# Optimization experiments

Hardware: AMD Instinct MI355X
Metric: run time of the kernel (lower is better)

The kernel has to match this reference:

```python
import jax, jax.numpy as jnp
import numpy as np

B, S, C = 2, 2048, 1024
U, H = 1024, 16
FFH = int(U * 4.0)
NEG = -1e9
EPS = 1e-5


def setup_inputs() -> dict:
    key = jax.random.key(0)
    ks = jax.random.split(key, 16)
    w = lambda k, sh: jax.random.normal(k, sh, dtype=jnp.float32) * 0.02
    return {
        'x': jax.random.normal(ks[0], (B, S, C), dtype=jnp.float32),
        'wq': w(ks[1], (C, U)), 'bq': jnp.zeros((U,), jnp.float32),
        'wk': w(ks[2], (C, U)), 'bk': jnp.zeros((U,), jnp.float32),
        'wv': w(ks[3], (C, U)), 'bv': jnp.zeros((U,), jnp.float32),
        'wf1': w(ks[4], (U, FFH)), 'bf1': jnp.zeros((FFH,), jnp.float32),
        'wf2': w(ks[5], (FFH, U)), 'bf2': jnp.zeros((U,), jnp.float32),
        'ln_g': jnp.ones((S, U), jnp.float32), 'ln_b': jnp.zeros((S, U), jnp.float32),
        'ffln_g': jnp.ones((S, U), jnp.float32), 'ffln_b': jnp.zeros((S, U), jnp.float32),
    }


def _ln2d(x, g, b):
    # LayerNorm over last two dims ([len_ts, units]) as in nn.LayerNorm([S, U])
    m = jnp.mean(x, axis=(-2, -1), keepdims=True)
    v = jnp.mean(jnp.square(x - m), axis=(-2, -1), keepdims=True)
    return (x - m) * jax.lax.rsqrt(v + EPS) * g + b


def reference(x, wq, bq, wk, bk, wv, bv, wf1, bf1, wf2, bf2, ln_g, ln_b, ffln_g, ffln_b):
    dh = U // H
    Q = (x @ wq + bq).reshape(B, S, H, dh)
    K = (x @ wk + bk).reshape(B, S, H, dh)
    V = (x @ wv + bv).reshape(B, S, H, dh)
    scores = jnp.einsum('bqhd,bkhd->bhqk', Q, K) / jnp.sqrt(jnp.float32(dh))
    mask = jnp.tril(jnp.ones((S, S), dtype=bool))  # causal tril buffer
    scores = jnp.where(mask, scores, NEG)
    attn = jax.nn.softmax(scores, axis=-1)
    out = jnp.einsum('bhqk,bkhd->bqhd', attn, V).reshape(B, S, U)
    out = out + x  # residual
    out = _ln2d(out, ln_g, ln_b)
    ff = jax.nn.relu(out @ wf1 + bf1) @ wf2 + bf2
    out = _ln2d(out + ff, ffln_g, ffln_b)
    return out
```

## Files before the change

kernel.cpp:

```cpp
#include <hip/hip_runtime.h>
#include <hip/hip_bf16.h>

typedef short s16x8 __attribute__((ext_vector_type(8)));
typedef float f32x4 __attribute__((ext_vector_type(4)));
typedef unsigned short u16x4 __attribute__((ext_vector_type(4)));

#define DEV static __device__ __forceinline__

DEV unsigned short f2bf(float f) {
  __hip_bfloat16 h = __float2bfloat16(f);
  return *reinterpret_cast<unsigned short*>(&h);
}
DEV float bf2f(unsigned short u) {
  union { unsigned u; float f; } v; v.u = (unsigned)u << 16; return v.f;
}

#define GLDS16(src, dst) \
  __builtin_amdgcn_global_load_lds((const __attribute__((address_space(1))) void*)(src), \
                                   (__attribute__((address_space(3))) void*)(dst), 16, 0, 0)

#define MFMA(a, b, c) __builtin_amdgcn_mfma_f32_16x16x32_bf16((a), (b), (c), 0, 0, 0)

__global__ __launch_bounds__(256) void k_f32_to_bf16(const float* __restrict__ in,
                                                     unsigned short* __restrict__ out, int n4) {
  int i = blockIdx.x * 256 + threadIdx.x;
  if (i >= n4) return;
  float4 v = ((const float4*)in)[i];
  u16x4 o; o.x = f2bf(v.x); o.y = f2bf(v.y); o.z = f2bf(v.z); o.w = f2bf(v.w);
  ((u16x4*)out)[i] = o;
}

__global__ __launch_bounds__(256) void k_transpose_w(const float* __restrict__ W,
                                                     unsigned short* __restrict__ Wt,
                                                     int K, int N, float scale) {
  __shared__ float t[64][65];
  int k0 = blockIdx.x * 64, n0 = blockIdx.y * 64;
  int tid = threadIdx.x;
#pragma unroll
  for (int i = 0; i < 16; ++i) {
    int idx = tid + i * 256; int r = idx >> 6, c = idx & 63;
    t[r][c] = W[(size_t)(k0 + r) * N + (n0 + c)];
  }
  __syncthreads();
#pragma unroll
  for (int i = 0; i < 16; ++i) {
    int idx = tid + i * 256; int r = idx >> 6, c = idx & 63;
    Wt[(size_t)(n0 + r) * K + (k0 + c)] = f2bf(t[c][r] * scale);
  }
}

__global__ void k_concat3(const float* __restrict__ a, const float* __restrict__ b,
                          const float* __restrict__ c, float* __restrict__ out, int n, float sa) {
  int i = blockIdx.x * 256 + threadIdx.x;
  if (i >= 3 * n) return;
  int j = (i < n) ? i : (i < 2 * n ? i - n : i - 2 * n);
  out[i] = (i < n) ? a[j] * sa : (i < 2 * n ? b[j] : c[j]);
}

template <int MODE>
__global__ __launch_bounds__(512, 2) void k_gemm8(
    const unsigned short* __restrict__ A, int lda,
    const unsigned short* __restrict__ Bt, int ldb,
    const float* __restrict__ bias,
    unsigned short* __restrict__ Cb, float* __restrict__ Cf, int ldc,
    int K, int nnt, size_t zstride) {
  __shared__ __align__(16) unsigned short As[2 * 2 * 8192];
  __shared__ __align__(16) unsigned short Bs[2 * 2 * 8192];
  int nwg = gridDim.x;
  int bid = blockIdx.x;
  int cpx = nwg >> 3;
  int swz = (bid & 7) * cpx + (bid >> 3);
  int mt = swz / nnt, nt = swz % nnt;
  int m0 = mt * 256, n0 = nt * 256;
  int tid = threadIdx.x, w = tid >> 6, l = tid & 63;
  int wm = (w >> 2) * 128, wn = (w & 3) * 64;
  int kb = blockIdx.z * K;

  int sr = tid >> 2;
  int gsrc = (tid & 3) ^ ((sr >> 1) & 3);
  const unsigned short* Ag0 = A + (size_t)(m0 + sr) * lda + kb + gsrc * 8;
  const unsigned short* Ag1 = Ag0 + (size_t)128 * lda;
  const unsigned short* Bg0 = Bt + (size_t)(n0 + sr) * ldb + kb + gsrc * 8;
  const unsigned short* Bg1 = Bg0 + (size_t)128 * ldb;

#define STG_A(t, kh) do { int _c = (t) * 64 + (kh) * 32; int _d = ((((t) & 1) * 2 + (kh)) * 8192); \
    GLDS16(Ag0 + _c, &As[_d + tid * 8]); GLDS16(Ag1 + _c, &As[_d + 4096 + tid * 8]); } while (0)
#define STG_B(t, kh) do { int _c = (t) * 64 + (kh) * 32; int _d = ((((t) & 1) * 2 + (kh)) * 8192); \
    GLDS16(Bg0 + _c, &Bs[_d + tid * 8]); GLDS16(Bg1 + _c, &Bs[_d + 4096 + tid * 8]); } while (0)

  int lswz = (l >> 1) & 3;
  int acol = ((l >> 4) ^ lswz) * 8;
  const unsigned short* Afr = &As[(wm + (l & 15)) * 32 + acol];
  const unsigned short* Bfr = &Bs[(wn + (l & 15)) * 32 + acol];

  f32x4 acc[8][4] = {};
  int nkt = K >> 6;

  STG_A(0, 0); STG_B(0, 0); STG_A(0, 1); STG_B(0, 1); STG_A(1, 0); STG_B(1, 0);
  asm volatile("s_waitcnt vmcnt(4)" ::: "memory");
  __builtin_amdgcn_s_barrier();
  __builtin_amdgcn_sched_barrier(0);

  for (int t = 0; t < nkt; ++t) {
    int cur = t & 1, rem = nkt - t;
    const unsigned short* ab = Afr + cur * 16384;
    const unsigned short* bb = Bfr + cur * 16384;
    s16x8 af[4], bf[4];
    if (t + 1 < nkt) STG_A(t + 1, 1);
#pragma unroll
    for (int nr = 0; nr < 4; ++nr) bf[nr] = *(const s16x8*)(bb + nr * 512);
#pragma unroll
    for (int mr = 0; mr < 4; ++mr) af[mr] = *(const s16x8*)(ab + mr * 512);
    __builtin_amdgcn_s_setprio(1);
#pragma unroll
    for (int mr = 0; mr < 4; ++mr)
#pragma unroll
      for (int nr = 0; nr < 4; ++nr)
        acc[mr][nr] = MFMA(af[mr], bf[nr], acc[mr][nr]);
    __builtin_amdgcn_s_setprio(0);
    if (t + 1 < nkt) STG_B(t + 1, 1);
#pragma unroll
    for (int mr = 0; mr < 4; ++mr) af[mr] = *(const s16x8*)(ab + 2048 + mr * 512);
    __builtin_amdgcn_s_setprio(1);
#pragma unroll
    for (int mr = 0; mr < 4; ++mr)
#pragma unroll
      for (int nr = 0; nr < 4; ++nr)
        acc[mr + 4][nr] = MFMA(af[mr], bf[nr], acc[mr + 4][nr]);
    __builtin_amdgcn_s_setprio(0);
    if (rem >= 2) { asm volatile("s_waitcnt vmcnt(4)" ::: "memory"); }
    else          { asm volatile("s_waitcnt vmcnt(0)" ::: "memory"); }
    __builtin_amdgcn_s_barrier();
    __builtin_amdgcn_sched_barrier(0);
    if (t + 2 < nkt) STG_A(t + 2, 0);
#pragma unroll
    for (int nr = 0; nr < 4; ++nr) bf[nr] = *(const s16x8*)(bb + 8192 + nr * 512);
#pragma unroll
    for (int mr = 0; mr < 4; ++mr) af[mr] = *(const s16x8*)(ab + 8192 + mr * 512);
    __builtin_amdgcn_s_setprio(1);
#pragma unroll
    for (int mr = 0; mr < 4; ++mr)
#pragma unroll
      for (int nr = 0; nr < 4; ++nr)
        acc[mr][nr] = MFMA(af[mr], bf[nr], acc[mr][nr]);
    __builtin_amdgcn_s_setprio(0);
    if (t + 2 < nkt) STG_B(t + 2, 0);
#pragma unroll
    for (int mr = 0; mr < 4; ++mr) af[mr] = *(const s16x8*)(ab + 8192 + 2048 + mr * 512);
    __builtin_amdgcn_s_setprio(1);
#pragma unroll
    for (int mr = 0; mr < 4; ++mr)
#pragma unroll
      for (int nr = 0; nr < 4; ++nr)
        acc[mr + 4][nr] = MFMA(af[mr], bf[nr], acc[mr + 4][nr]);
    __builtin_amdgcn_s_setprio(0);
    if (rem >= 3) { asm volatile("s_waitcnt vmcnt(4)" ::: "memory"); }
    else          { asm volatile("s_waitcnt vmcnt(0)" ::: "memory"); }
    __builtin_amdgcn_s_barrier();
    __builtin_amdgcn_sched_barrier(0);
  }
#undef STG_A
#undef STG_B

  unsigned short* Cbz = (MODE == 3) ? (Cb + zstride * blockIdx.z) : Cb;
#pragma unroll
  for (int mr = 0; mr < 8; ++mr) {
    int rb = m0 + wm + mr * 16 + (l >> 4) * 4;
#pragma unroll
    for (int nr = 0; nr < 4; ++nr) {
      int col = n0 + wn + nr * 16 + (l & 15);
      float bv = (MODE == 3) ? 0.f : bias[col];
#pragma unroll
      for (int j = 0; j < 4; ++j) {
        float v = acc[mr][nr][j] + bv;
        size_t off = (size_t)(rb + j) * ldc + col;
        if (MODE == 1) v = fmaxf(v, 0.f);
        Cbz[off] = f2bf(v);
      }
    }
  }
}

__global__ __launch_bounds__(256) void k_ff2_reduce(
    unsigned short* __restrict__ slices, const float* __restrict__ bias,
    const unsigned short* __restrict__ resid, float* __restrict__ partials) {
  __shared__ float red[8];
  int i = blockIdx.x;
  size_t rb = (size_t)i * 4096;
  int c = threadIdx.x * 4;
  u16x4 a0 = *(const u16x4*)(slices + rb + c);
  u16x4 a1 = *(const u16x4*)(slices + rb + 1024 + c);
  u16x4 a2 = *(const u16x4*)(slices + rb + 2048 + c);
  u16x4 a3 = *(const u16x4*)(slices + rb + 3072 + c);
  float4 bv = *(const float4*)(bias + c);
  u16x4 rv = *(const u16x4*)(resid + (size_t)i * 1024 + c);
  float4 o;
  o.x = bf2f(a0.x) + bf2f(a1.x) + bf2f(a2.x) + bf2f(a3.x) + bv.x + bf2f(rv.x);
  o.y = bf2f(a0.y) + bf2f(a1.y) + bf2f(a2.y) + bf2f(a3.y) + bv.y + bf2f(rv.y);
  o.z = bf2f(a0.z) + bf2f(a1.z) + bf2f(a2.z) + bf2f(a3.z) + bv.z + bf2f(rv.z);
  o.w = bf2f(a0.w) + bf2f(a1.w) + bf2f(a2.w) + bf2f(a3.w) + bv.w + bf2f(rv.w);
  __syncthreads();
  *(float4*)((float*)slices + (size_t)i * 2048 + c) = o;
  float bsum = o.x + o.y + o.z + o.w;
  float bsq = o.x * o.x + o.y * o.y + o.z * o.z + o.w * o.w;
  int wv = threadIdx.x >> 6, lv = threadIdx.x & 63;
#pragma unroll
  for (int mk = 1; mk < 64; mk <<= 1) { bsum += __shfl_xor(bsum, mk); bsq += __shfl_xor(bsq, mk); }
  if (lv == 0) { red[wv] = bsum; red[4 + wv] = bsq; }
  __syncthreads();
  if (threadIdx.x == 0) {
    partials[i * 2] = red[0] + red[1] + red[2] + red[3];
    partials[i * 2 + 1] = red[4] + red[5] + red[6] + red[7];
  }
}

__global__ __launch_bounds__(256) void k_transpose_v(const unsigned short* __restrict__ V, int ldv,
                                                     unsigned short* __restrict__ Vt, int S, int H) {
  __shared__ __align__(16) unsigned short t[64][72];
  int s0 = blockIdx.x * 64;
  int bh = blockIdx.y; int b = bh / H, h = bh % H;
  const unsigned short* src = V + (size_t)(b * S) * ldv + h * 64;
  unsigned short* dst = Vt + (size_t)bh * 64 * S;
  int tid = threadIdx.x;
#pragma unroll
  for (int i = 0; i < 2; ++i) {
    int idx = tid + i * 256;
    int s = idx >> 3, c = (idx & 7) * 8;
    s16x8 v = *(const s16x8*)(src + (size_t)(s0 + s) * ldv + c);
#pragma unroll
    for (int j = 0; j < 8; ++j) t[c + j][s] = (unsigned short)v[j];
  }
  __syncthreads();
#pragma unroll
  for (int i = 0; i < 2; ++i) {
    int idx = tid + i * 256;
    int d = idx >> 3, c = (idx & 7) * 8;
    *(s16x8*)(dst + (size_t)d * S + s0 + c) = *(const s16x8*)&t[d][c];
  }
}

__global__ __launch_bounds__(256) void k_attn(
    const unsigned short* __restrict__ Qg, const unsigned short* __restrict__ Kg,
    const unsigned short* __restrict__ Vt, int ldqk,
    const float* __restrict__ x, unsigned short* __restrict__ hpre,
    float* __restrict__ partials, int S, int H) {
  __shared__ __align__(16) unsigned short Ks[2][64 * 64];
  __shared__ __align__(16) unsigned short Vs[2][64 * 64];
  __shared__ __align__(16) unsigned short Ps[4][16 * 64];
  int bh = blockIdx.x, b = bh >> 4, h = bh & 15;
  const int nqt = S / 64;
  int qt = nqt - 1 - (int)blockIdx.y;
  int tid = threadIdx.x, w = tid >> 6, l = tid & 63;
  const int U = H * 64;
  const unsigned short* Qb = Qg + (size_t)(b * S) * ldqk + h * 64;
  const unsigned short* Kb = Kg + (size_t)(b * S) * ldqk + h * 64;
  const unsigned short* Vb = Vt + (size_t)bh * 64 * S;
  const float* xb = x + (size_t)(b * S) * U + h * 64;
  unsigned short* hb = hpre + (size_t)(b * S) * U + h * 64;
  int sg_r[2], sg_c[2];
#pragma unroll
  for (int it = 0; it < 2; ++it) {
    int g = it * 256 + tid;
    sg_r[it] = g >> 3;
    sg_c[it] = ((g & 7) ^ ((g >> 3) & 7)) * 8;
  }
  unsigned short* Pw = &Ps[w][0];
  int qloc = l & 15;
  int kloc = (l >> 4) * 4;

  int qrow = qt * 64 + w * 16 + qloc;
  s16x8 qf0 = *(const s16x8*)(Qb + (size_t)qrow * ldqk + (l >> 4) * 8);
  s16x8 qf1 = *(const s16x8*)(Qb + (size_t)qrow * ldqk + 32 + (l >> 4) * 8);
  f32x4 o[4] = {};
  float m = -1e30f, lsum = 0.f;

#pragma unroll
  for (int it = 0; it < 2; ++it) {
    GLDS16(Kb + (size_t)sg_r[it] * ldqk + sg_c[it], &Ks[0][(it * 256 + tid) * 8]);
    GLDS16(Vb + (size_t)sg_r[it] * S + sg_c[it], &Vs[0][(it * 256 + tid) * 8]);
  }

  for (int kt = 0; kt <= qt; ++kt) {
    int cur = kt & 1;
    __syncthreads();
    if (kt < qt) {
      int nb = cur ^ 1, kn = (kt + 1) * 64;
#pragma unroll
      for (int it = 0; it < 2; ++it) {
        GLDS16(Kb + (size_t)(kn + sg_r[it]) * ldqk + sg_c[it], &Ks[nb][(it * 256 + tid) * 8]);
        GLDS16(Vb + (size_t)sg_r[it] * S + kn + sg_c[it], &Vs[nb][(it * 256 + tid) * 8]);
      }
    }
    f32x4 sc[4];
    __builtin_amdgcn_s_setprio(1);
#pragma unroll
    for (int fn = 0; fn < 4; ++fn) {
      int row = fn * 16 + (l & 15);
      s16x8 kf0 = *(const s16x8*)&Ks[cur][row * 64 + ((((l >> 4)) ^ (row & 7)) * 8)];
      s16x8 kf1 = *(const s16x8*)&Ks[cur][row * 64 + (((4 + (l >> 4)) ^ (row & 7)) * 8)];
      f32x4 z = {};
      z = MFMA(kf0, qf0, z);
      z = MFMA(kf1, qf1, z);
      sc[fn] = z;
    }
    __builtin_amdgcn_s_setprio(0);
    if (kt == qt) {
      int qsel = w * 16 + qloc;
#pragma unroll
      for (int fn = 0; fn < 4; ++fn)
#pragma unroll
        for (int j = 0; j < 4; ++j)
          if (fn * 16 + kloc + j > qsel) sc[fn][j] = -1e30f;
    }
    float mx = sc[0][0];
#pragma unroll
    for (int fn = 0; fn < 4; ++fn)
#pragma unroll
      for (int j = 0; j < 4; ++j) mx = fmaxf(mx, sc[fn][j]);
    mx = fmaxf(mx, __shfl_xor(mx, 16));
    mx = fmaxf(mx, __shfl_xor(mx, 32));
    if (__ballot(mx > m + 11.5415603f)) {
      float mnew = fmaxf(m, mx);
      float alpha = exp2f(m - mnew);
      m = mnew;
      lsum *= alpha;
#pragma unroll
      for (int j = 0; j < 4; ++j) {
        float aj = __shfl(alpha, (l & 48) | (kloc + j));
#pragma unroll
        for (int fd = 0; fd < 4; ++fd) o[fd][j] *= aj;
      }
    }
    float rs = 0.f;
#pragma unroll
    for (int fn = 0; fn < 4; ++fn) {
      u16x4 pk;
#pragma unroll
      for (int j = 0; j < 4; ++j) {
        float p = exp2f(sc[fn][j] - m);
        rs += p;
        ((unsigned short*)&pk)[j] = f2bf(p);
      }
      int kb2 = fn * 16 + kloc;
      int el = qloc * 64 + (((kb2 >> 3) ^ (qloc & 7)) * 8) + (kb2 & 7);
      *(u16x4*)&Pw[el] = pk;
    }
    rs += __shfl_xor(rs, 16);
    rs += __shfl_xor(rs, 32);
    lsum += rs;
    __builtin_amdgcn_s_setprio(1);
#pragma unroll
    for (int kk = 0; kk < 2; ++kk) {
      int prow = l & 15;
      s16x8 pa = *(const s16x8*)&Pw[prow * 64 + (((kk * 4 + (l >> 4)) ^ (prow & 7)) * 8)];
#pragma unroll
      for (int fd = 0; fd < 4; ++fd) {
        int vrow = fd * 16 + (l & 15);
        s16x8 vf = *(const s16x8*)&Vs[cur][vrow * 64 + (((kk * 4 + (l >> 4)) ^ (vrow & 7)) * 8)];
        o[fd] = MFMA(pa, vf, o[fd]);
      }
    }
    __builtin_amdgcn_s_setprio(0);
  }
  float bsum = 0.f, bsq = 0.f;
#pragma unroll
  for (int j = 0; j < 4; ++j) {
    float lr = __shfl(lsum, (l & 48) | (kloc + j));
    float inv = 1.f / lr;
    int row = qt * 64 + w * 16 + kloc + j;
#pragma unroll
    for (int fd = 0; fd < 4; ++fd) {
      int col = fd * 16 + (l & 15);
      float v = o[fd][j] * inv + xb[(size_t)row * U + col];
      hb[(size_t)row * U + col] = f2bf(v);
      bsum += v; bsq += v * v;
    }
  }
#pragma unroll
  for (int mk = 1; mk < 64; mk <<= 1) { bsum += __shfl_xor(bsum, mk); bsq += __shfl_xor(bsq, mk); }
  if (l == 0) { float* r = (float*)&Ps[w][0]; r[0] = bsum; r[1] = bsq; }
  __syncthreads();
  if (tid == 0) {
    float s2 = 0.f, q2 = 0.f;
#pragma unroll
    for (int ww = 0; ww < 4; ++ww) { const float* r = (const float*)&Ps[ww][0]; s2 += r[0]; q2 += r[1]; }
    int pi = b * (H * nqt) + h * nqt + qt;
    partials[pi * 2] = s2; partials[pi * 2 + 1] = q2;
  }
}

__global__ __launch_bounds__(256) void k_ln_stats(const float* __restrict__ partials, int nper,
                                                  float* __restrict__ stats, float invN) {
  int b = blockIdx.x, tid = threadIdx.x;
  float s = 0.f, q = 0.f;
  for (int i = tid; i < nper; i += 256) { s += partials[(b * nper + i) * 2]; q += partials[(b * nper + i) * 2 + 1]; }
#pragma unroll
  for (int mk = 1; mk < 64; mk <<= 1) { s += __shfl_xor(s, mk); q += __shfl_xor(q, mk); }
  __shared__ float red[8];
  int w = tid >> 6, l = tid & 63;
  if (l == 0) { red[w] = s; red[4 + w] = q; }
  __syncthreads();
  if (tid == 0) {
    s = red[0] + red[1] + red[2] + red[3];
    q = red[4] + red[5] + red[6] + red[7];
    float m = s * invN, var = q * invN - m * m;
    stats[b * 2] = m; stats[b * 2 + 1] = rsqrtf(var + 1e-5f);
  }
}

__global__ __launch_bounds__(256) void k_ln_apply_b(
    const unsigned short* __restrict__ src, const float* __restrict__ stats,
    const float* __restrict__ g, const float* __restrict__ bt,
    unsigned short* __restrict__ outb, int SU) {
  int b = blockIdx.y;
  int idx = (blockIdx.x * 256 + threadIdx.x) * 4;
  float m = stats[b * 2], r = stats[b * 2 + 1];
  u16x4 v4 = *(const u16x4*)(src + (size_t)b * SU + idx);
  float4 gg = *(const float4*)(g + idx);
  float4 bb = *(const float4*)(bt + idx);
  u16x4 ob;
  ob.x = f2bf((bf2f(v4.x) - m) * r * gg.x + bb.x);
  ob.y = f2bf((bf2f(v4.y) - m) * r * gg.y + bb.y);
  ob.z = f2bf((bf2f(v4.z) - m) * r * gg.z + bb.z);
  ob.w = f2bf((bf2f(v4.w) - m) * r * gg.w + bb.w);
  *(u16x4*)(outb + (size_t)b * SU + idx) = ob;
}

__global__ __launch_bounds__(256) void k_ln_apply2(
    const float* __restrict__ src, const float* __restrict__ stats,
    const float* __restrict__ g, const float* __restrict__ bt,
    float* __restrict__ outf) {
  int b = blockIdx.y;
  int row = blockIdx.x;
  int grow = b * 2048 + row;
  int c = threadIdx.x * 4;
  float m = stats[b * 2], r = stats[b * 2 + 1];
  float4 v = *(const float4*)(src + (size_t)grow * 2048 + c);
  float4 gg = *(const float4*)(g + (size_t)row * 1024 + c);
  float4 bb = *(const float4*)(bt + (size_t)row * 1024 + c);
  float4 o;
  o.x = (v.x - m) * r * gg.x + bb.x;
  o.y = (v.y - m) * r * gg.y + bb.y;
  o.z = (v.z - m) * r * gg.z + bb.z;
  o.w = (v.w - m) * r * gg.w + bb.w;
  *(float4*)(outf + (size_t)grow * 1024 + c) = o;
}

extern "C" void kernel_launch(void* const* d_in, const int* in_sizes, int n_in,
                              void* d_out, int out_size, void* d_ws, size_t ws_size,
                              hipStream_t stream) {
  (void)in_sizes; (void)n_in; (void)out_size; (void)ws_size;
  const int S = 2048, H = 16;
  const float* x   = (const float*)d_in[0];
  const float* wq  = (const float*)d_in[1];
  const float* bq  = (const float*)d_in[2];
  const float* wk  = (const float*)d_in[3];
  const float* bk  = (const float*)d_in[4];
  const float* wv  = (const float*)d_in[5];
  const float* bv  = (const float*)d_in[6];
  const float* wf1 = (const float*)d_in[7];
  const float* bf1 = (const float*)d_in[8];
  const float* wf2 = (const float*)d_in[9];
  const float* bf2 = (const float*)d_in[10];
  const float* lng = (const float*)d_in[11];
  const float* lnb = (const float*)d_in[12];
  const float* ffg = (const float*)d_in[13];
  const float* ffb = (const float*)d_in[14];

  char* ws = (char*)d_ws;
  unsigned short* wqkvT = (unsigned short*)(ws);
  unsigned short* wf1T  = (unsigned short*)(ws + 6291456);
  unsigned short* wf2T  = (unsigned short*)(ws + 14680064);
  unsigned short* xb    = (unsigned short*)(ws + 23068672);
  unsigned short* qkv   = (unsigned short*)(ws + 31457280);
  unsigned short* vt    = (unsigned short*)(ws + 56623104);
  unsigned short* h1b   = (unsigned short*)(ws + 65011712);
  unsigned short* hpreb = (unsigned short*)(ws + 73400320);
  unsigned short* ff2s  = (unsigned short*)(ws + 73400320);
  unsigned short* f1b   = (unsigned short*)(ws + 23068672);
  float* biasqkv        = (float*)(ws + 106954752);
  float* part_attn      = (float*)(ws + 106967040);
  float* stats1         = (float*)(ws + 106977280);
  float* ffpart2        = (float*)(ws);
  float* stats2         = (float*)(ws + 65536);

  const float qscale = 0.125f * 1.44269504f;
  k_f32_to_bf16<<<4096, 256, 0, stream>>>(x, xb, 4096 * 1024 / 4);
  k_transpose_w<<<dim3(16, 16), 256, 0, stream>>>(wq, wqkvT, 1024, 1024, qscale);
  k_transpose_w<<<dim3(16, 16), 256, 0, stream>>>(wk, wqkvT + 1024 * 1024, 1024, 1024, 1.0f);
  k_transpose_w<<<dim3(16, 16), 256, 0, stream>>>(wv, wqkvT + 2048 * 1024, 1024, 1024, 1.0f);
  k_transpose_w<<<dim3(16, 64), 256, 0, stream>>>(wf1, wf1T, 1024, 4096, 1.0f);
  k_transpose_w<<<dim3(64, 16), 256, 0, stream>>>(wf2, wf2T, 4096, 1024, 1.0f);
  k_concat3<<<12, 256, 0, stream>>>(bq, bk, bv, biasqkv, 1024, qscale);

  k_gemm8<0><<<dim3(192, 1, 1), 512, 0, stream>>>(xb, 1024, wqkvT, 1024, biasqkv,
      qkv, nullptr, 3072, 1024, 12, 0);

  k_transpose_v<<<dim3(32, 32), 256, 0, stream>>>(qkv + 2048, 3072, vt, S, H);

  k_attn<<<dim3(32, 32), 256, 0, stream>>>(qkv, qkv + 1024, vt, 3072, x, hpreb, part_attn, S, H);

  k_ln_stats<<<2, 256, 0, stream>>>(part_attn, 512, stats1, 1.f / (2048.f * 1024.f));
  k_ln_apply_b<<<dim3(2048, 2), 256, 0, stream>>>(hpreb, stats1, lng, lnb, h1b, S * 1024);

  k_gemm8<1><<<dim3(256, 1, 1), 512, 0, stream>>>(h1b, 1024, wf1T, 1024, bf1,
      f1b, nullptr, 4096, 1024, 16, 0);

  k_gemm8<3><<<dim3(64, 1, 4), 512, 0, stream>>>(f1b, 4096, wf2T, 4096, nullptr,
      ff2s, nullptr, 4096, 1024, 4, 1024);

  k_ff2_reduce<<<4096, 256, 0, stream>>>(ff2s, bf2, h1b, ffpart2);

  k_ln_stats<<<2, 256, 0, stream>>>(ffpart2, 2048, stats2, 1.f / (2048.f * 1024.f));
  k_ln_apply2<<<dim3(2048, 2), 256, 0, stream>>>((float*)ff2s, stats2, ffg, ffb, (float*)d_out);
}
```

Measured before the change: 236.2 us.

## Fuse V transpose into QKV GEMM epilogue and use 32x32 MFMA attention

The QKV GEMM gets a new epilogue mode that writes Q and K into separate contiguous buffers and writes V already transposed per head, with a permuted sequence order, so the separate V transpose kernel is dropped. The attention kernel is rewritten to use 2 waves of 128 threads, each covering 32 query rows with 32x32x16 MFMAs. P stays in registers as the A operand instead of going through LDS, and the hardware exp2 is used directly. This removes a launch and an extra pass over V, and cuts LDS traffic for P. In exchange the V stores are scattered 8-byte writes and the attention blocks have fewer threads each.

```diff
diff --git a/kernel.cpp b/kernel.cpp
--- a/kernel.cpp
+++ b/kernel.cpp
@@ -3,7 +3,9 @@
 
 typedef short s16x8 __attribute__((ext_vector_type(8)));
 typedef float f32x4 __attribute__((ext_vector_type(4)));
+typedef float f32x16 __attribute__((ext_vector_type(16)));
 typedef unsigned short u16x4 __attribute__((ext_vector_type(4)));
+typedef unsigned u32x4 __attribute__((ext_vector_type(4)));
 
 #define DEV static __device__ __forceinline__
 
@@ -20,6 +22,7 @@
                                    (__attribute__((address_space(3))) void*)(dst), 16, 0, 0)
 
 #define MFMA(a, b, c) __builtin_amdgcn_mfma_f32_16x16x32_bf16((a), (b), (c), 0, 0, 0)
+#define MFMA32(a, b, c) __builtin_amdgcn_mfma_f32_32x32x16_bf16((a), (b), (c), 0, 0, 0)
 
 __global__ __launch_bounds__(256) void k_f32_to_bf16(const float* __restrict__ in,
                                                      unsigned short* __restrict__ out, int n4) {
@@ -63,7 +66,9 @@
     const unsigned short* __restrict__ Bt, int ldb,
     const float* __restrict__ bias,
     unsigned short* __restrict__ Cb, float* __restrict__ Cf, int ldc,
-    int K, int nnt, size_t zstride) {
+    int K, int nnt, size_t zstride,
+    unsigned short* __restrict__ Cq, unsigned short* __restrict__ Ck,
+    unsigned short* __restrict__ Cv) {
   __shared__ __align__(16) unsigned short As[2 * 2 * 8192];
   __shared__ __align__(16) unsigned short Bs[2 * 2 * 8192];
   int nwg = gridDim.x;
@@ -162,6 +167,41 @@
 #undef STG_A
 #undef STG_B
 
+  if (MODE == 4) {
+    if (nt < 8) {
+      unsigned short* dst = (nt < 4) ? Cq : Ck;
+      int cb = (nt < 4) ? 0 : 1024;
+#pragma unroll
+      for (int mr = 0; mr < 8; ++mr) {
+        int rb = m0 + wm + mr * 16 + (l >> 4) * 4;
+#pragma unroll
+        for (int nr = 0; nr < 4; ++nr) {
+          int col = n0 + wn + nr * 16 + (l & 15);
+          float bv = bias[col];
+#pragma unroll
+          for (int j = 0; j < 4; ++j)
+            dst[(size_t)(rb + j) * 1024 + (col - cb)] = f2bf(acc[mr][nr][j] + bv);
+        }
+      }
+    } else {
+#pragma unroll
+      for (int mr = 0; mr < 8; ++mr) {
+        int rb = m0 + wm + mr * 16 + (l >> 4) * 4;
+        int b2 = rb >> 11, s2 = rb & 2047;
+        int s2p = (s2 & ~12) | ((s2 & 4) << 1) | ((s2 & 8) >> 1);
+#pragma unroll
+        for (int nr = 0; nr < 4; ++nr) {
+          int col2 = n0 - 2048 + wn + nr * 16 + (l & 15);
+          float bv = bias[col2 + 2048];
+          u16x4 pk;
+#pragma unroll
+          for (int j = 0; j < 4; ++j) ((unsigned short*)&pk)[j] = f2bf(acc[mr][nr][j] + bv);
+          *(u16x4*)(Cv + ((size_t)((b2 * 16 + (col2 >> 6)) * 64 + (col2 & 63))) * 2048 + s2p) = pk;
+        }
+      }
+    }
+    return;
+  }
   unsigned short* Cbz = (MODE == 3) ? (Cb + zstride * blockIdx.z) : Cb;
 #pragma unroll
   for (int mr = 0; mr < 8; ++mr) {
@@ -214,70 +254,49 @@
   }
 }
 
-__global__ __launch_bounds__(256) void k_transpose_v(const unsigned short* __restrict__ V, int ldv,
-                                                     unsigned short* __restrict__ Vt, int S, int H) {
-  __shared__ __align__(16) unsigned short t[64][72];
-  int s0 = blockIdx.x * 64;
-  int bh = blockIdx.y; int b = bh / H, h = bh % H;
-  const unsigned short* src = V + (size_t)(b * S) * ldv + h * 64;
-  unsigned short* dst = Vt + (size_t)bh * 64 * S;
-  int tid = threadIdx.x;
-#pragma unroll
-  for (int i = 0; i < 2; ++i) {
-    int idx = tid + i * 256;
-    int s = idx >> 3, c = (idx & 7) * 8;
-    s16x8 v = *(const s16x8*)(src + (size_t)(s0 + s) * ldv + c);
-#pragma unroll
-    for (int j = 0; j < 8; ++j) t[c + j][s] = (unsigned short)v[j];
-  }
-  __syncthreads();
-#pragma unroll
-  for (int i = 0; i < 2; ++i) {
-    int idx = tid + i * 256;
-    int d = idx >> 3, c = (idx & 7) * 8;
-    *(s16x8*)(dst + (size_t)d * S + s0 + c) = *(const s16x8*)&t[d][c];
-  }
-}
-
-__global__ __launch_bounds__(256) void k_attn(
+__global__ __launch_bounds__(128, 2) void k_attn(
     const unsigned short* __restrict__ Qg, const unsigned short* __restrict__ Kg,
-    const unsigned short* __restrict__ Vt, int ldqk,
+    const unsigned short* __restrict__ Vt,
     const float* __restrict__ x, unsigned short* __restrict__ hpre,
     float* __restrict__ partials, int S, int H) {
-  __shared__ __align__(16) unsigned short Ks[2][64 * 64];
-  __shared__ __align__(16) unsigned short Vs[2][64 * 64];
-  __shared__ __align__(16) unsigned short Ps[4][16 * 64];
+  __shared__ __align__(16) unsigned short Ks[2][4096];
+  __shared__ __align__(16) unsigned short Vs[2][4096];
+  __shared__ float ascr[2][32];
+  __shared__ float red[4];
   int bh = blockIdx.x, b = bh >> 4, h = bh & 15;
   const int nqt = S / 64;
   int qt = nqt - 1 - (int)blockIdx.y;
   int tid = threadIdx.x, w = tid >> 6, l = tid & 63;
+  int lo = l & 31, hi5 = l >> 5;
   const int U = H * 64;
-  const unsigned short* Qb = Qg + (size_t)(b * S) * ldqk + h * 64;
-  const unsigned short* Kb = Kg + (size_t)(b * S) * ldqk + h * 64;
+  const unsigned short* Qb = Qg + (size_t)(b * S) * 1024 + h * 64;
+  const unsigned short* Kb = Kg + (size_t)(b * S) * 1024 + h * 64;
   const unsigned short* Vb = Vt + (size_t)bh * 64 * S;
-  const float* xb = x + (size_t)(b * S) * U + h * 64;
-  unsigned short* hb = hpre + (size_t)(b * S) * U + h * 64;
-  int sg_r[2], sg_c[2];
-#pragma unroll
-  for (int it = 0; it < 2; ++it) {
-    int g = it * 256 + tid;
+
+  int sg_r[4], sg_c[4];
+#pragma unroll
+  for (int it = 0; it < 4; ++it) {
+    int g = it * 128 + tid;
     sg_r[it] = g >> 3;
     sg_c[it] = ((g & 7) ^ ((g >> 3) & 7)) * 8;
   }
-  unsigned short* Pw = &Ps[w][0];
-  int qloc = l & 15;
-  int kloc = (l >> 4) * 4;
-
-  int qrow = qt * 64 + w * 16 + qloc;
-  s16x8 qf0 = *(const s16x8*)(Qb + (size_t)qrow * ldqk + (l >> 4) * 8);
-  s16x8 qf1 = *(const s16x8*)(Qb + (size_t)qrow * ldqk + 32 + (l >> 4) * 8);
-  f32x4 o[4] = {};
+  int qrow = qt * 64 + w * 32 + lo;
+  s16x8 qf[4];
+#pragma unroll
+  for (int s = 0; s < 4; ++s)
+    qf[s] = *(const s16x8*)(Qb + (size_t)qrow * 1024 + s * 16 + hi5 * 8);
+
+  int krow[16];
+#pragma unroll
+  for (int r = 0; r < 16; ++r) krow[r] = (r & 3) + 8 * (r >> 2) + 4 * hi5;
+
+  f32x16 o0 = {}, o1 = {};
   float m = -1e30f, lsum = 0.f;
 
 #pragma unroll
-  for (int it = 0; it < 2; ++it) {
-    GLDS16(Kb + (size_t)sg_r[it] * ldqk + sg_c[it], &Ks[0][(it * 256 + tid) * 8]);
-    GLDS16(Vb + (size_t)sg_r[it] * S + sg_c[it], &Vs[0][(it * 256 + tid) * 8]);
+  for (int it = 0; it < 4; ++it) {
+    GLDS16(Kb + (size_t)sg_r[it] * 1024 + sg_c[it], &Ks[0][(it * 128 + tid) * 8]);
+    GLDS16(Vb + (size_t)sg_r[it] * S + sg_c[it], &Vs[0][(it * 128 + tid) * 8]);
   }
 
   for (int kt = 0; kt <= qt; ++kt) {
@@ -286,106 +305,103 @@
     if (kt < qt) {
       int nb = cur ^ 1, kn = (kt + 1) * 64;
 #pragma unroll
-      for (int it = 0; it < 2; ++it) {
-        GLDS16(Kb + (size_t)(kn + sg_r[it]) * ldqk + sg_c[it], &Ks[nb][(it * 256 + tid) * 8]);
-        GLDS16(Vb + (size_t)sg_r[it] * S + kn + sg_c[it], &Vs[nb][(it * 256 + tid) * 8]);
+      for (int it = 0; it < 4; ++it) {
+        GLDS16(Kb + (size_t)(kn + sg_r[it]) * 1024 + sg_c[it], &Ks[nb][(it * 128 + tid) * 8]);
+        GLDS16(Vb + (size_t)sg_r[it] * S + kn + sg_c[it], &Vs[nb][(it * 128 + tid) * 8]);
       }
     }
-    f32x4 sc[4];
+    f32x16 sc0 = {}, sc1 = {};
     __builtin_amdgcn_s_setprio(1);
 #pragma unroll
-    for (int fn = 0; fn < 4; ++fn) {
-      int row = fn * 16 + (l & 15);
-      s16x8 kf0 = *(const s16x8*)&Ks[cur][row * 64 + ((((l >> 4)) ^ (row & 7)) * 8)];
-      s16x8 kf1 = *(const s16x8*)&Ks[cur][row * 64 + (((4 + (l >> 4)) ^ (row & 7)) * 8)];
-      f32x4 z = {};
-      z = MFMA(kf0, qf0, z);
-      z = MFMA(kf1, qf1, z);
-      sc[fn] = z;
+    for (int s = 0; s < 4; ++s) {
+      int gc = ((2 * s + hi5) ^ (lo & 7)) * 8;
+      s16x8 kf0 = *(const s16x8*)&Ks[cur][lo * 64 + gc];
+      s16x8 kf1 = *(const s16x8*)&Ks[cur][(32 + lo) * 64 + gc];
+      sc0 = MFMA32(kf0, qf[s], sc0);
+      sc1 = MFMA32(kf1, qf[s], sc1);
     }
     __builtin_amdgcn_s_setprio(0);
     if (kt == qt) {
-      int qsel = w * 16 + qloc;
-#pragma unroll
-      for (int fn = 0; fn < 4; ++fn)
-#pragma unroll
-        for (int j = 0; j < 4; ++j)
-          if (fn * 16 + kloc + j > qsel) sc[fn][j] = -1e30f;
-    }
-    float mx = sc[0][0];
-#pragma unroll
-    for (int fn = 0; fn < 4; ++fn)
-#pragma unroll
-      for (int j = 0; j < 4; ++j) mx = fmaxf(mx, sc[fn][j]);
-    mx = fmaxf(mx, __shfl_xor(mx, 16));
+      int wq = w * 32 + lo;
+#pragma unroll
+      for (int r = 0; r < 16; ++r) {
+        if (krow[r] > wq) sc0[r] = -1e30f;
+        if (krow[r] + 32 > wq) sc1[r] = -1e30f;
+      }
+    }
+    float mx = sc0[0];
+#pragma unroll
+    for (int r = 1; r < 16; ++r) mx = fmaxf(mx, sc0[r]);
+#pragma unroll
+    for (int r = 0; r < 16; ++r) mx = fmaxf(mx, sc1[r]);
     mx = fmaxf(mx, __shfl_xor(mx, 32));
     if (__ballot(mx > m + 11.5415603f)) {
       float mnew = fmaxf(m, mx);
-      float alpha = exp2f(m - mnew);
+      float alpha = __builtin_amdgcn_exp2f(m - mnew);
       m = mnew;
       lsum *= alpha;
-#pragma unroll
-      for (int j = 0; j < 4; ++j) {
-        float aj = __shfl(alpha, (l & 48) | (kloc + j));
-#pragma unroll
-        for (int fd = 0; fd < 4; ++fd) o[fd][j] *= aj;
+      if (l < 32) ascr[w][lo] = alpha;
+#pragma unroll
+      for (int r = 0; r < 16; ++r) {
+        float aj = ascr[w][krow[r]];
+        o0[r] *= aj; o1[r] *= aj;
       }
     }
     float rs = 0.f;
-#pragma unroll
-    for (int fn = 0; fn < 4; ++fn) {
-      u16x4 pk;
-#pragma unroll
-      for (int j = 0; j < 4; ++j) {
-        float p = exp2f(sc[fn][j] - m);
-        rs += p;
-        ((unsigned short*)&pk)[j] = f2bf(p);
-      }
-      int kb2 = fn * 16 + kloc;
-      int el = qloc * 64 + (((kb2 >> 3) ^ (qloc & 7)) * 8) + (kb2 & 7);
-      *(u16x4*)&Pw[el] = pk;
-    }
-    rs += __shfl_xor(rs, 16);
+    unsigned wk0[8], wk1[8];
+#pragma unroll
+    for (int j = 0; j < 8; ++j) {
+      float p0 = __builtin_amdgcn_exp2f(sc0[2 * j] - m);
+      float p1 = __builtin_amdgcn_exp2f(sc0[2 * j + 1] - m);
+      rs += p0 + p1;
+      wk0[j] = (unsigned)f2bf(p0) | ((unsigned)f2bf(p1) << 16);
+      float p2 = __builtin_amdgcn_exp2f(sc1[2 * j] - m);
+      float p3 = __builtin_amdgcn_exp2f(sc1[2 * j + 1] - m);
+      rs += p2 + p3;
+      wk1[j] = (unsigned)f2bf(p2) | ((unsigned)f2bf(p3) << 16);
+    }
     rs += __shfl_xor(rs, 32);
     lsum += rs;
     __builtin_amdgcn_s_setprio(1);
 #pragma unroll
-    for (int kk = 0; kk < 2; ++kk) {
-      int prow = l & 15;
-      s16x8 pa = *(const s16x8*)&Pw[prow * 64 + (((kk * 4 + (l >> 4)) ^ (prow & 7)) * 8)];
-#pragma unroll
-      for (int fd = 0; fd < 4; ++fd) {
-        int vrow = fd * 16 + (l & 15);
-        s16x8 vf = *(const s16x8*)&Vs[cur][vrow * 64 + (((kk * 4 + (l >> 4)) ^ (vrow & 7)) * 8)];
-        o[fd] = MFMA(pa, vf, o[fd]);
-      }
+    for (int s = 0; s < 4; ++s) {
+      u32x4 paw;
+      if (s == 0)      { paw.x = wk0[0]; paw.y = wk0[1]; paw.z = wk0[2]; paw.w = wk0[3]; }
+      else if (s == 1) { paw.x = wk0[4]; paw.y = wk0[5]; paw.z = wk0[6]; paw.w = wk0[7]; }
+      else if (s == 2) { paw.x = wk1[0]; paw.y = wk1[1]; paw.z = wk1[2]; paw.w = wk1[3]; }
+      else             { paw.x = wk1[4]; paw.y = wk1[5]; paw.z = wk1[6]; paw.w = wk1[7]; }
+      s16x8 pa = *(s16x8*)&paw;
+      int gc = ((2 * s + hi5) ^ (lo & 7)) * 8;
+      s16x8 vf0 = *(const s16x8*)&Vs[cur][lo * 64 + gc];
+      s16x8 vf1 = *(const s16x8*)&Vs[cur][(32 + lo) * 64 + gc];
+      o0 = MFMA32(pa, vf0, o0);
+      o1 = MFMA32(pa, vf1, o1);
     }
     __builtin_amdgcn_s_setprio(0);
   }
+  if (l < 32) ascr[w][lo] = 1.f / lsum;
   float bsum = 0.f, bsq = 0.f;
-#pragma unroll
-  for (int j = 0; j < 4; ++j) {
-    float lr = __shfl(lsum, (l & 48) | (kloc + j));
-    float inv = 1.f / lr;
-    int row = qt * 64 + w * 16 + kloc + j;
-#pragma unroll
-    for (int fd = 0; fd < 4; ++fd) {
-      int col = fd * 16 + (l & 15);
-      float v = o[fd][j] * inv + xb[(size_t)row * U + col];
-      hb[(size_t)row * U + col] = f2bf(v);
-      bsum += v; bsq += v * v;
-    }
+  unsigned short* hb = hpre + (size_t)(b * S) * U + h * 64;
+  const float* xb = x + (size_t)(b * S) * U + h * 64;
+#pragma unroll
+  for (int r = 0; r < 16; ++r) {
+    float inv = ascr[w][krow[r]];
+    int srow = qt * 64 + w * 32 + krow[r];
+    size_t base = (size_t)srow * U + lo;
+    float v0 = o0[r] * inv + xb[base];
+    float v1 = o1[r] * inv + xb[base + 32];
+    hb[base] = f2bf(v0);
+    hb[base + 32] = f2bf(v1);
+    bsum += v0 + v1; bsq += v0 * v0 + v1 * v1;
   }
 #pragma unroll
   for (int mk = 1; mk < 64; mk <<= 1) { bsum += __shfl_xor(bsum, mk); bsq += __shfl_xor(bsq, mk); }
-  if (l == 0) { float* r = (float*)&Ps[w][0]; r[0] = bsum; r[1] = bsq; }
+  if (l == 0) { red[w * 2] = bsum; red[w * 2 + 1] = bsq; }
   __syncthreads();
   if (tid == 0) {
-    float s2 = 0.f, q2 = 0.f;
-#pragma unroll
-    for (int ww = 0; ww < 4; ++ww) { const float* r = (const float*)&Ps[ww][0]; s2 += r[0]; q2 += r[1]; }
     int pi = b * (H * nqt) + h * nqt + qt;
-    partials[pi * 2] = s2; partials[pi * 2 + 1] = q2;
+    partials[pi * 2] = red[0] + red[2];
+    partials[pi * 2 + 1] = red[1] + red[3];
   }
 }
 
@@ -472,7 +488,8 @@
   unsigned short* wf1T  = (unsigned short*)(ws + 6291456);
   unsigned short* wf2T  = (unsigned short*)(ws + 14680064);
   unsigned short* xb    = (unsigned short*)(ws + 23068672);
-  unsigned short* qkv   = (unsigned short*)(ws + 31457280);
+  unsigned short* qb    = (unsigned short*)(ws + 31457280);
+  unsigned short* kbuf  = (unsigned short*)(ws + 39845888);
   unsigned short* vt    = (unsigned short*)(ws + 56623104);
   unsigned short* h1b   = (unsigned short*)(ws + 65011712);
   unsigned short* hpreb = (unsigned short*)(ws + 73400320);
@@ -493,21 +510,19 @@
   k_transpose_w<<<dim3(64, 16), 256, 0, stream>>>(wf2, wf2T, 4096, 1024, 1.0f);
   k_concat3<<<12, 256, 0, stream>>>(bq, bk, bv, biasqkv, 1024, qscale);
 
-  k_gemm8<0><<<dim3(192, 1, 1), 512, 0, stream>>>(xb, 1024, wqkvT, 1024, biasqkv,
-      qkv, nullptr, 3072, 1024, 12, 0);
-
-  k_transpose_v<<<dim3(32, 32), 256, 0, stream>>>(qkv + 2048, 3072, vt, S, H);
-
-  k_attn<<<dim3(32, 32), 256, 0, stream>>>(qkv, qkv + 1024, vt, 3072, x, hpreb, part_attn, S, H);
+  k_gemm8<4><<<dim3(192, 1, 1), 512, 0, stream>>>(xb, 1024, wqkvT, 1024, biasqkv,
+      nullptr, nullptr, 0, 1024, 12, 0, qb, kbuf, vt);
+
+  k_attn<<<dim3(32, 32), 128, 0, stream>>>(qb, kbuf, vt, x, hpreb, part_attn, S, H);
 
   k_ln_stats<<<2, 256, 0, stream>>>(part_attn, 512, stats1, 1.f / (2048.f * 1024.f));
   k_ln_apply_b<<<dim3(2048, 2), 256, 0, stream>>>(hpreb, stats1, lng, lnb, h1b, S * 1024);
 
   k_gemm8<1><<<dim3(256, 1, 1), 512, 0, stream>>>(h1b, 1024, wf1T, 1024, bf1,
-      f1b, nullptr, 4096, 1024, 16, 0);
+      f1b, nullptr, 4096, 1024, 16, 0, nullptr, nullptr, nullptr);
 
   k_gemm8<3><<<dim3(64, 1, 4), 512, 0, stream>>>(f1b, 4096, wf2T, 4096, nullptr,
-      ff2s, nullptr, 4096, 1024, 4, 1024);
+      ff2s, nullptr, 4096, 1024, 4, 1024, nullptr, nullptr, nullptr);
 
   k_ff2_reduce<<<4096, 256, 0, stream>>>(ff2s, bf2, h1b, ffpart2);
 
```

New measurement: 236.4 us. About the same (+0.1%).
